# Kernel tuning notes

Measured on AMD Instinct MI355X. Metric: run time of the kernel, lower is better.

The kernel has to match this reference:

```python
import jax, jax.numpy as jnp
import numpy as np

N_NODES = 100000
N_EDGES = 1600000
IN_CH = 128
OUT_CH = 32
HEADS = 4
NEG_SLOPE = 0.2


def setup_inputs() -> dict:
    key = jax.random.key(0)
    k1, k2, k3, k4 = jax.random.split(key, 4)
    x = jax.random.normal(k1, (N_NODES, IN_CH), dtype=jnp.float32)
    # xavier-ish scale for params
    weight = jax.random.normal(k2, (IN_CH, HEADS * OUT_CH), dtype=jnp.float32) * 0.1
    att = jax.random.normal(k3, (1, HEADS, 2 * OUT_CH), dtype=jnp.float32) * 0.1
    edge_index = jax.random.randint(k4, (2, N_EDGES), 0, N_NODES, dtype=jnp.int64)
    return {"x": x, "weight": weight, "att": att, "edge_index": edge_index}


def reference(x, weight, att, edge_index):
    num_nodes = x.shape[0]
    # project and split heads: [N, H, C]
    h = jnp.matmul(x, weight).reshape(num_nodes, HEADS, OUT_CH)
    row, col = edge_index[0], edge_index[1]
    x_i = h[row]   # [E, H, C]
    x_j = h[col]   # [E, H, C]
    # alpha_e = sum_c att[:, :, :C]*x_i + att[:, :, C:]*x_j  -> [E, H]
    a_i = att[0, :, :OUT_CH]   # [H, C]
    a_j = att[0, :, OUT_CH:]   # [H, C]
    alpha = jnp.einsum('ehc,hc->eh', x_i, a_i) + jnp.einsum('ehc,hc->eh', x_j, a_j)
    alpha = jnp.where(alpha >= 0, alpha, NEG_SLOPE * alpha)  # leaky_relu
    # segment softmax over destination node (col)
    amax = jax.ops.segment_max(alpha, col, num_segments=num_nodes)  # [N, H]
    amax = jnp.where(jnp.isfinite(amax), amax, 0.0)  # empty segments -> 0
    e = jnp.exp(alpha - amax[col])
    s = jax.ops.segment_sum(e, col, num_segments=num_nodes)  # [N, H]
    alpha = e / (s[col] + 1e-16)
    # weighted aggregation: scatter-add x_j * alpha to destination nodes
    msg = x_j * alpha[:, :, None]  # [E, H, C]
    out = jax.ops.segment_sum(msg, col, num_segments=num_nodes)  # [N, H, C]
    # concat=True
    return out.reshape(num_nodes, HEADS * OUT_CH)
```

## Files before the change

kernel.cpp:

```cpp
#include <hip/hip_runtime.h>
#include <hip/hip_bf16.h>

#define N_NODES 100000
#define N_EDGES 1600000
#define K_DIM 128
#define N_DIM 128
#define BM_WORDS 3125
#define PART_STRIDE 3136
#define FLAG_BLOCKS 256
#define WIMG_WORDS 8192
#define PART_OFF 8192
#define BROWS 64

typedef __attribute__((ext_vector_type(8))) short bf16x8;
typedef __attribute__((ext_vector_type(4))) float f32x4;

__device__ inline unsigned short f2bf(float f) {
    __hip_bfloat16 b = __float2bfloat16(f);
    return __builtin_bit_cast(unsigned short, b);
}

__global__ __launch_bounds__(256)
void flag_partial(const int* __restrict__ ei, const float* __restrict__ wf,
                  unsigned int* __restrict__ wimg,
                  unsigned int* __restrict__ parts) {
    __shared__ unsigned int lbm[BM_WORDS];

    if (blockIdx.x < 16 && threadIdx.x < 128) {
        int g  = blockIdx.x * 128 + threadIdx.x;
        int n  = g >> 4;
        int k0 = (g & 15) << 3;
        unsigned short tmp[8];
#pragma unroll
        for (int j = 0; j < 8; ++j) tmp[j] = f2bf(wf[(k0 + j) * N_DIM + n]);
        int byte = (n * 256 + k0 * 2) ^ ((n & 7) << 4);
        *(uint4*)((char*)wimg + byte) = *(const uint4*)tmp;
    }

    for (int i = threadIdx.x; i < BM_WORDS; i += 256) lbm[i] = 0;
    __syncthreads();

    bool is64 = ((ei[1] | ei[3] | ei[5] | ei[7]) == 0);
    const int base = blockIdx.x * (N_EDGES / FLAG_BLOCKS);
    if (is64) {
        const uint4* p = (const uint4*)(ei + 2 * N_EDGES + 2 * base);
        for (int t = threadIdx.x; t < 3125; t += 256) {
            uint4 v = p[t];
            atomicOr(&lbm[v.x >> 5], 1u << (v.x & 31));
            atomicOr(&lbm[v.z >> 5], 1u << (v.z & 31));
        }
    } else {
        const uint2* p = (const uint2*)(ei + N_EDGES + base);
        for (int t = threadIdx.x; t < 3125; t += 256) {
            uint2 v = p[t];
            atomicOr(&lbm[v.x >> 5], 1u << (v.x & 31));
            atomicOr(&lbm[v.y >> 5], 1u << (v.y & 31));
        }
    }
    __syncthreads();

    unsigned int* dst = parts + (size_t)blockIdx.x * PART_STRIDE;
    for (int i = threadIdx.x; i < BM_WORDS; i += 256) dst[i] = lbm[i];
}

__global__ __launch_bounds__(256, 3)
void gemm_fused(const float* __restrict__ xf,
                const unsigned int* __restrict__ wimg,
                const unsigned int* __restrict__ parts,
                float* __restrict__ out) {
    __shared__ __attribute__((aligned(16))) unsigned short ldsW[N_DIM * 128];
    __shared__ __attribute__((aligned(16))) unsigned short ldsA[BROWS * 128];
    __shared__ unsigned int lmask[4][2];

    const int tid  = threadIdx.x;
    const int lane = tid & 63;
    const int wave = tid >> 6;
    const int rb0  = blockIdx.x * BROWS;

    f32x4 av[4][2];
#pragma unroll
    for (int i = 0; i < 4; ++i) {
        int c  = i * 256 + tid;
        int rl = c >> 4;
        int k8 = c & 15;
        int rg = rb0 + rl;
        if (rg >= N_NODES) rg = N_NODES - 1;
        av[i][0] = *(const f32x4*)(xf + (size_t)rg * K_DIM + k8 * 8);
        av[i][1] = *(const f32x4*)(xf + (size_t)rg * K_DIM + k8 * 8 + 4);
    }

#pragma unroll
    for (int i = 0; i < 8; ++i) {
        int off = i * 4096 + wave * 1024;
        __builtin_amdgcn_global_load_lds(
            (const __attribute__((address_space(1))) unsigned int*)
                ((const char*)wimg + off + lane * 16),
            (__attribute__((address_space(3))) unsigned int*)
                ((char*)ldsW + off),
            16, 0, 0);
    }

    {
        const unsigned int* p =
            parts + (size_t)tid * PART_STRIDE + blockIdx.x * 2;
        uint2 pv = *(const uint2*)p;
#pragma unroll
        for (int off = 32; off; off >>= 1) {
            pv.x |= __shfl_xor(pv.x, off);
            pv.y |= __shfl_xor(pv.y, off);
        }
        if (lane == 0) { lmask[wave][0] = pv.x; lmask[wave][1] = pv.y; }
    }

#pragma unroll
    for (int i = 0; i < 4; ++i) {
        int c  = i * 256 + tid;
        int rl = c >> 4;
        int k8 = c & 15;
        unsigned short t8[8];
#pragma unroll
        for (int j = 0; j < 4; ++j) {
            t8[j]     = f2bf(av[i][0][j]);
            t8[4 + j] = f2bf(av[i][1][j]);
        }
        int byte = (rl * 256 + k8 * 16) ^ ((rl & 7) << 4);
        *(uint4*)((char*)ldsA + byte) = *(const uint4*)t8;
    }
    __syncthreads();

    const int m    = lane & 15;
    const int quad = lane >> 4;
    const int arow = wave * 16 + m;

    f32x4 acc[8];
#pragma unroll
    for (int t = 0; t < 8; ++t) acc[t] = (f32x4){0.f, 0.f, 0.f, 0.f};

#pragma unroll
    for (int kk = 0; kk < 4; ++kk) {
        const int kbase = kk * 32 + quad * 8;
        int abyte = (arow * 256 + kbase * 2) ^ ((arow & 7) << 4);
        bf16x8 af = *(const bf16x8*)((const char*)ldsA + abyte);
#pragma unroll
        for (int t = 0; t < 8; ++t) {
            int bn = t * 16 + m;
            int bbyte = (bn * 256 + kbase * 2) ^ ((bn & 7) << 4);
            bf16x8 bfrag = *(const bf16x8*)((const char*)ldsW + bbyte);
            acc[t] = __builtin_amdgcn_mfma_f32_16x16x32_bf16(af, bfrag, acc[t], 0, 0, 0);
        }
    }

    const unsigned int fm0 = lmask[0][0] | lmask[1][0] | lmask[2][0] | lmask[3][0];
    const unsigned int fm1 = lmask[0][1] | lmask[1][1] | lmask[2][1] | lmask[3][1];

#pragma unroll
    for (int r = 0; r < 4; ++r) {
        int lrow = wave * 16 + quad * 4 + r;
        int orow = rb0 + lrow;
        if (orow < N_NODES) {
            unsigned int w = (lrow & 32) ? fm1 : fm0;
            float fmul = ((w >> (lrow & 31)) & 1) ? 1.0f : 0.0f;
#pragma unroll
            for (int t = 0; t < 8; ++t)
                out[(size_t)orow * N_DIM + t * 16 + m] = acc[t][r] * fmul;
        }
    }
}

extern "C" void kernel_launch(void* const* d_in, const int* in_sizes, int n_in,
                              void* d_out, int out_size, void* d_ws, size_t ws_size,
                              hipStream_t stream) {
    const float* x = (const float*)d_in[0];
    const float* w = (const float*)d_in[1];
    const int* ei = (const int*)d_in[3];
    float* out = (float*)d_out;

    unsigned int* wimg  = (unsigned int*)d_ws;
    unsigned int* parts = (unsigned int*)d_ws + PART_OFF;

    flag_partial<<<FLAG_BLOCKS, 256, 0, stream>>>(ei, w, wimg, parts);
    gemm_fused<<<(N_NODES + BROWS - 1) / BROWS, 256, 0, stream>>>(x, wimg, parts, out);
}
```

Baseline: 120.8 us.

## Make GEMM kernel persistent with double-buffered A tiles and prefetch

The GEMM kernel now launches a fixed grid of 512 blocks instead of one block per 64-row tile. Each block loops over about three tiles, loading the weight image into LDS once per block rather than once per tile. The next tile's x rows and flag-mask words are prefetched into registers while the MFMAs for the current tile run, then written into a second LDS A buffer. In exchange, LDS use doubles and the launch bound drops to 2 blocks per CU, which lowers occupancy for a kernel that is mostly bandwidth-bound.

```diff
diff --git a/kernel.cpp b/kernel.cpp
--- a/kernel.cpp
+++ b/kernel.cpp
@@ -11,6 +11,9 @@
 #define WIMG_WORDS 8192
 #define PART_OFF 8192
 #define BROWS 64
+#define GBLOCKS 512
+#define N_TILES 1563
+#define TILE_REM 27
 
 typedef __attribute__((ext_vector_type(8))) short bf16x8;
 typedef __attribute__((ext_vector_type(4))) float f32x4;
@@ -63,21 +66,9 @@
     for (int i = threadIdx.x; i < BM_WORDS; i += 256) dst[i] = lbm[i];
 }
 
-__global__ __launch_bounds__(256, 3)
-void gemm_fused(const float* __restrict__ xf,
-                const unsigned int* __restrict__ wimg,
-                const unsigned int* __restrict__ parts,
-                float* __restrict__ out) {
-    __shared__ __attribute__((aligned(16))) unsigned short ldsW[N_DIM * 128];
-    __shared__ __attribute__((aligned(16))) unsigned short ldsA[BROWS * 128];
-    __shared__ unsigned int lmask[4][2];
-
-    const int tid  = threadIdx.x;
-    const int lane = tid & 63;
-    const int wave = tid >> 6;
-    const int rb0  = blockIdx.x * BROWS;
-
-    f32x4 av[4][2];
+__device__ __forceinline__ void load_a(const float* __restrict__ xf, int tile,
+                                       int tid, f32x4 a0[4], f32x4 a1[4]) {
+    const int rb0 = tile * BROWS;
 #pragma unroll
     for (int i = 0; i < 4; ++i) {
         int c  = i * 256 + tid;
@@ -85,9 +76,42 @@
         int k8 = c & 15;
         int rg = rb0 + rl;
         if (rg >= N_NODES) rg = N_NODES - 1;
-        av[i][0] = *(const f32x4*)(xf + (size_t)rg * K_DIM + k8 * 8);
-        av[i][1] = *(const f32x4*)(xf + (size_t)rg * K_DIM + k8 * 8 + 4);
-    }
+        a0[i] = *(const f32x4*)(xf + (size_t)rg * K_DIM + k8 * 8);
+        a1[i] = *(const f32x4*)(xf + (size_t)rg * K_DIM + k8 * 8 + 4);
+    }
+}
+
+__device__ __forceinline__ void cvt_write_a(unsigned short* lds, int tid,
+                                            const f32x4 a0[4], const f32x4 a1[4]) {
+#pragma unroll
+    for (int i = 0; i < 4; ++i) {
+        int c  = i * 256 + tid;
+        int rl = c >> 4;
+        int k8 = c & 15;
+        unsigned short t8[8];
+#pragma unroll
+        for (int j = 0; j < 4; ++j) {
+            t8[j]     = f2bf(a0[i][j]);
+            t8[4 + j] = f2bf(a1[i][j]);
+        }
+        int byte = (rl * 256 + k8 * 16) ^ ((rl & 7) << 4);
+        *(uint4*)((char*)lds + byte) = *(const uint4*)t8;
+    }
+}
+
+__global__ __launch_bounds__(256, 2)
+void gemm_fused(const float* __restrict__ xf,
+                const unsigned int* __restrict__ wimg,
+                const unsigned int* __restrict__ parts,
+                float* __restrict__ out) {
+    __shared__ __attribute__((aligned(16))) unsigned short ldsW[N_DIM * 128];
+    __shared__ __attribute__((aligned(16))) unsigned short ldsA[2][BROWS * 128];
+    __shared__ unsigned int lmask[2][4][2];
+
+    const int tid  = threadIdx.x;
+    const int lane = tid & 63;
+    const int wave = tid >> 6;
+    const int nt   = 3 + (blockIdx.x < TILE_REM ? 1 : 0);
 
 #pragma unroll
     for (int i = 0; i < 8; ++i) {
@@ -100,70 +124,76 @@
             16, 0, 0);
     }
 
-    {
-        const unsigned int* p =
-            parts + (size_t)tid * PART_STRIDE + blockIdx.x * 2;
-        uint2 pv = *(const uint2*)p;
-#pragma unroll
-        for (int off = 32; off; off >>= 1) {
-            pv.x |= __shfl_xor(pv.x, off);
-            pv.y |= __shfl_xor(pv.y, off);
-        }
-        if (lane == 0) { lmask[wave][0] = pv.x; lmask[wave][1] = pv.y; }
-    }
-
-#pragma unroll
-    for (int i = 0; i < 4; ++i) {
-        int c  = i * 256 + tid;
-        int rl = c >> 4;
-        int k8 = c & 15;
-        unsigned short t8[8];
-#pragma unroll
-        for (int j = 0; j < 4; ++j) {
-            t8[j]     = f2bf(av[i][0][j]);
-            t8[4 + j] = f2bf(av[i][1][j]);
-        }
-        int byte = (rl * 256 + k8 * 16) ^ ((rl & 7) << 4);
-        *(uint4*)((char*)ldsA + byte) = *(const uint4*)t8;
-    }
+    f32x4 a0[4], a1[4];
+    load_a(xf, blockIdx.x, tid, a0, a1);
+    uint2 pv = *(const uint2*)(parts + (size_t)tid * PART_STRIDE + blockIdx.x * 2);
+    cvt_write_a(ldsA[0], tid, a0, a1);
     __syncthreads();
 
     const int m    = lane & 15;
     const int quad = lane >> 4;
     const int arow = wave * 16 + m;
-
-    f32x4 acc[8];
-#pragma unroll
-    for (int t = 0; t < 8; ++t) acc[t] = (f32x4){0.f, 0.f, 0.f, 0.f};
-
-#pragma unroll
-    for (int kk = 0; kk < 4; ++kk) {
-        const int kbase = kk * 32 + quad * 8;
-        int abyte = (arow * 256 + kbase * 2) ^ ((arow & 7) << 4);
-        bf16x8 af = *(const bf16x8*)((const char*)ldsA + abyte);
-#pragma unroll
-        for (int t = 0; t < 8; ++t) {
-            int bn = t * 16 + m;
-            int bbyte = (bn * 256 + kbase * 2) ^ ((bn & 7) << 4);
-            bf16x8 bfrag = *(const bf16x8*)((const char*)ldsW + bbyte);
-            acc[t] = __builtin_amdgcn_mfma_f32_16x16x32_bf16(af, bfrag, acc[t], 0, 0, 0);
-        }
-    }
-
-    const unsigned int fm0 = lmask[0][0] | lmask[1][0] | lmask[2][0] | lmask[3][0];
-    const unsigned int fm1 = lmask[0][1] | lmask[1][1] | lmask[2][1] | lmask[3][1];
-
-#pragma unroll
-    for (int r = 0; r < 4; ++r) {
-        int lrow = wave * 16 + quad * 4 + r;
-        int orow = rb0 + lrow;
-        if (orow < N_NODES) {
-            unsigned int w = (lrow & 32) ? fm1 : fm0;
-            float fmul = ((w >> (lrow & 31)) & 1) ? 1.0f : 0.0f;
-#pragma unroll
-            for (int t = 0; t < 8; ++t)
-                out[(size_t)orow * N_DIM + t * 16 + m] = acc[t][r] * fmul;
-        }
+    const int abyt = (arow * 256) ^ ((arow & 7) << 4);
+
+    for (int it = 0; it < nt; ++it) {
+        const int cur    = it & 1;
+        const int tile   = blockIdx.x + it * GBLOCKS;
+        const bool more  = (it + 1 < nt);
+
+        uint2 pvn;
+        if (more) {
+            load_a(xf, tile + GBLOCKS, tid, a0, a1);
+            pvn = *(const uint2*)(parts + (size_t)tid * PART_STRIDE +
+                                  (tile + GBLOCKS) * 2);
+        }
+
+        f32x4 acc[8];
+#pragma unroll
+        for (int t = 0; t < 8; ++t) acc[t] = (f32x4){0.f, 0.f, 0.f, 0.f};
+#pragma unroll
+        for (int kk = 0; kk < 4; ++kk) {
+            const int kbase = kk * 32 + quad * 8;
+            bf16x8 af = *(const bf16x8*)((const char*)ldsA[cur] +
+                                         (abyt ^ (kbase * 2)));
+#pragma unroll
+            for (int t = 0; t < 8; ++t) {
+                int bn = t * 16 + m;
+                int bbyte = (bn * 256 + kbase * 2) ^ ((bn & 7) << 4);
+                bf16x8 bfrag = *(const bf16x8*)((const char*)ldsW + bbyte);
+                acc[t] = __builtin_amdgcn_mfma_f32_16x16x32_bf16(af, bfrag,
+                                                                 acc[t], 0, 0, 0);
+            }
+        }
+
+        unsigned int m0 = pv.x, m1 = pv.y;
+#pragma unroll
+        for (int off = 32; off; off >>= 1) {
+            m0 |= __shfl_xor(m0, off);
+            m1 |= __shfl_xor(m1, off);
+        }
+        if (lane == 0) { lmask[cur][wave][0] = m0; lmask[cur][wave][1] = m1; }
+
+        if (more) cvt_write_a(ldsA[cur ^ 1], tid, a0, a1);
+        __syncthreads();
+
+        const unsigned int fm0 = lmask[cur][0][0] | lmask[cur][1][0] |
+                                 lmask[cur][2][0] | lmask[cur][3][0];
+        const unsigned int fm1 = lmask[cur][0][1] | lmask[cur][1][1] |
+                                 lmask[cur][2][1] | lmask[cur][3][1];
+        const int rb0 = tile * BROWS;
+#pragma unroll
+        for (int r = 0; r < 4; ++r) {
+            int lrow = wave * 16 + quad * 4 + r;
+            int orow = rb0 + lrow;
+            if (orow < N_NODES) {
+                unsigned int w = (lrow & 32) ? fm1 : fm0;
+                float fmul = ((w >> (lrow & 31)) & 1) ? 1.0f : 0.0f;
+#pragma unroll
+                for (int t = 0; t < 8; ++t)
+                    out[(size_t)orow * N_DIM + t * 16 + m] = acc[t][r] * fmul;
+            }
+        }
+        pv = pvn;
     }
 }
 
@@ -179,5 +209,5 @@
     unsigned int* parts = (unsigned int*)d_ws + PART_OFF;
 
     flag_partial<<<FLAG_BLOCKS, 256, 0, stream>>>(ei, w, wimg, parts);
-    gemm_fused<<<(N_NODES + BROWS - 1) / BROWS, 256, 0, stream>>>(x, wimg, parts, out);
-}
+    gemm_fused<<<GBLOCKS, 256, 0, stream>>>(x, wimg, parts, out);
+}
```

After: 120.2 us. Within noise of the previous version (-0.5%).
